# Kernel tuning notes

Measured on AMD Instinct MI355X. Metric: run time of the kernel, lower is better.

The kernel has to match this reference:

```python
import jax, jax.numpy as jnp
import numpy as np

N_NODES, N_EDGES, N_REL, F_DIM, N_HEAD, N_LAYERS = 20000, 100000, 1000, 128, 4, 4
NEG_SLOPE = 0.2  # PyG GATv2Conv default negative_slope


def _gatv2_layer(x, ea_full, src, dst, Wl, bl, Wr, br, We, att, bias):
    # x: [N, F]; ea_full: [Etot, F] edge attrs (incl. self-loop rows)
    N = x.shape[0]
    H, C = att.shape  # heads, out-dim per head
    xl = (x @ Wl + bl).reshape(N, H, C)          # source-side projection
    xr = (x @ Wr + br).reshape(N, H, C)          # target-side projection
    ee = (ea_full @ We).reshape(-1, H, C)        # [Etot, H, C] edge embedding
    # GATv2 scoring: leaky_relu(x_i + x_j + e) . att
    e = jax.nn.leaky_relu(xl[src] + xr[dst] + ee, NEG_SLOPE)
    logits = jnp.einsum('ehc,hc->eh', e, att)    # [Etot, H]
    # segment softmax over edges grouped by destination node
    m = jax.ops.segment_max(logits, dst, num_segments=N)
    p = jnp.exp(logits - m[dst])
    denom = jax.ops.segment_sum(p, dst, num_segments=N)
    alpha = p / denom[dst]                       # [Etot, H]
    out = jax.ops.segment_sum(alpha[:, :, None] * xl[src], dst, num_segments=N)
    return out.mean(axis=1) + bias               # concat=False -> head mean


def setup_inputs() -> dict:
    key = jax.random.key(0)
    ks = jax.random.split(key, 12)
    N, E, R, F, H, L = N_NODES, N_EDGES, N_REL, F_DIM, N_HEAD, N_LAYERS
    HC = H * F
    s = 1.0 / np.sqrt(F)
    return {
        'x': jax.random.normal(ks[0], (N, F), jnp.float32),
        'edge_index': jax.random.randint(ks[1], (2, E), 0, N, dtype=jnp.int32),
        'relations': jax.random.normal(ks[2], (R, F), jnp.float32),
        'relation_index': jax.random.randint(ks[3], (E,), 0, R, dtype=jnp.int32),
        'Wl': jax.random.normal(ks[4], (L, F, HC), jnp.float32) * s,
        'bl': jnp.zeros((L, HC), jnp.float32),
        'Wr': jax.random.normal(ks[5], (L, F, HC), jnp.float32) * s,
        'br': jnp.zeros((L, HC), jnp.float32),
        'We': jax.random.normal(ks[6], (L, F, HC), jnp.float32) * s,
        'att': jax.random.normal(ks[7], (L, H, F), jnp.float32) * s,
        'bias': jnp.zeros((L, F), jnp.float32),
    }


def reference(x, edge_index, relations, relation_index, Wl, bl, Wr, br, We, att, bias):
    N = x.shape[0]
    sl = jnp.arange(N, dtype=edge_index.dtype)
    src = jnp.concatenate([edge_index[0], sl])   # add_self_loops=True
    dst = jnp.concatenate([edge_index[1], sl])
    ea = relations[relation_index]               # [E, F]
    # self-loop edge_attr uses fill_value='mean' (PyG default)
    ea_mean = ea.mean(axis=0)
    ea_full = jnp.concatenate([ea, jnp.broadcast_to(ea_mean, (N, ea.shape[1]))])
    h = x
    for l in range(N_LAYERS):
        h = _gatv2_layer(h, ea_full, src, dst, Wl[l], bl[l], Wr[l], br[l], We[l], att[l], bias[l])
    return (h, relations)
```

## Files before the change

kernel.cpp:

```cpp
#include <hip/hip_runtime.h>
#include <hip/hip_bf16.h>

#define N_NODES   20000
#define N_EDGES   100000
#define N_REL     1000
#define F_DIM     128
#define N_HEAD    4
#define HC        512
#define HC2       256
#define N_LAYERS  4
#define REL_EXT_ROWS 1008
#define NEG_SLOPE 0.2f
#define NODE_MB   ((N_NODES + 63) / 64)
#define REL_MB    ((REL_EXT_ROWS + 63) / 64)

typedef __attribute__((ext_vector_type(8))) short short8;
typedef __attribute__((ext_vector_type(4))) float floatx4;

__device__ __forceinline__ float loadIn(const void* p, size_t i, int f32) {
    if (f32) return ((const float*)p)[i];
    union { unsigned int u; float f; } c;
    c.u = ((unsigned int)((const unsigned short*)p)[i]) << 16;
    return c.f;
}

__device__ __forceinline__ unsigned short f2bf(float v) {
    __hip_bfloat16 b = __float2bfloat16(v);
    return *(unsigned short*)&b;
}

__device__ __forceinline__ void unpack2(unsigned int u, float& lo, float& hi) {
    union { unsigned int u; float f; } a, b;
    a.u = u << 16;
    b.u = u & 0xFFFF0000u;
    lo = a.f; hi = b.f;
}

__device__ __forceinline__ void unpack8(uint4 v, float* f) {
    unpack2(v.x, f[0], f[1]);
    unpack2(v.y, f[2], f[3]);
    unpack2(v.z, f[4], f[5]);
    unpack2(v.w, f[6], f[7]);
}

__global__ void detect_kernel(const unsigned short* __restrict__ x, int* __restrict__ flag) {
    int t = threadIdx.x;
    int cnt = 0;
    for (int j = t; j < 256; j += 64) {
        int e = (x[j] >> 7) & 0xFF;
        if (e >= 143) cnt++;
    }
    for (int off = 32; off; off >>= 1) cnt += __shfl_xor(cnt, off);
    if (t == 0) flag[0] = (cnt >= 8) ? 1 : 0;
}


__global__ void hist_kernel(const int* __restrict__ dst, const int* __restrict__ rel,
                            int* __restrict__ deg, int* __restrict__ rcount) {
    int e = blockIdx.x * 256 + threadIdx.x;
    if (e < N_EDGES) {
        atomicAdd(&deg[dst[e]], 1);
        atomicAdd(&rcount[rel[e]], 1);
    }
}

__global__ void ea_mean_kernel(const int* __restrict__ rcount,
                               const void* __restrict__ relations,
                               float* __restrict__ ea_mean, const int* __restrict__ flag) {
    int f32 = flag[0];
    int b = blockIdx.x;
    int t = threadIdx.x;
    int col = t & 127;
    int rhalf = t >> 7;
    float acc = 0.f;
    for (int j = 0; j < 4; ++j) {
        int r = b * 8 + j * 2 + rhalf;
        acc += (float)rcount[r] * loadIn(relations, (size_t)r * F_DIM + col, f32);
    }
    __shared__ float part[256];
    part[t] = acc;
    __syncthreads();
    if (t < 128)
        atomicAdd(&ea_mean[col], (part[t] + part[t + 128]) * (1.f / (float)N_EDGES));
}

__global__ void relext_kernel(const void* __restrict__ relations,
                              const float* __restrict__ ea_mean,
                              unsigned short* __restrict__ rel_ext, const int* __restrict__ flag) {
    int idx = blockIdx.x * 256 + threadIdx.x;
    if (idx >= REL_EXT_ROWS * F_DIM) return;
    int f32 = flag[0];
    int r = idx >> 7;
    int c = idx & 127;
    float v;
    if (r < N_REL)       v = loadIn(relations, idx, f32);
    else if (r == N_REL) v = ea_mean[c];
    else                 v = 0.f;
    rel_ext[idx] = f2bf(v);
}

__global__ void scan_kernel(const int* __restrict__ deg,
                            int* __restrict__ row_start, int* __restrict__ cursor) {
    __shared__ int part[1024];
    int t = threadIdx.x;
    const int CH = (N_NODES + 1023) / 1024;
    int base = t * CH;
    int sum = 0;
    for (int j = 0; j < CH; ++j) {
        int idx = base + j;
        if (idx < N_NODES) sum += deg[idx];
    }
    part[t] = sum;
    __syncthreads();
    for (int off = 1; off < 1024; off <<= 1) {
        int u = (t >= off) ? part[t - off] : 0;
        __syncthreads();
        part[t] += u;
        __syncthreads();
    }
    int run = part[t] - sum;
    for (int j = 0; j < CH; ++j) {
        int idx = base + j;
        if (idx < N_NODES) {
            row_start[idx] = run;
            cursor[idx] = run;
            run += deg[idx];
        }
    }
    if (t == 1023) row_start[N_NODES] = part[1023];
}

__global__ void scatter_kernel(const int* __restrict__ src, const int* __restrict__ dst,
                               const int* __restrict__ rel, int* __restrict__ cursor,
                               int* __restrict__ csr_pack) {
    int e = blockIdx.x * 256 + threadIdx.x;
    if (e < N_EDGES) {
        int d = dst[e];
        int p = atomicAdd(&cursor[d], 1);
        csr_pack[p] = src[e] | (rel[e] << 16);
    }
}

__global__ void tail_kernel(const void* __restrict__ relations, void* __restrict__ out,
                            const int* __restrict__ flag) {
    int i = blockIdx.x * 256 + threadIdx.x;
    if (i >= N_REL * F_DIM) return;
    int f32 = flag[0];
    float v = loadIn(relations, i, f32);
    size_t o = (size_t)N_NODES * F_DIM + i;
    if (f32) ((float*)out)[o] = v;
    else     ((unsigned short*)out)[o] = f2bf(v);
}

__global__ void w_transpose_kernel(const void* __restrict__ Wl, const void* __restrict__ Wr,
                                   const void* __restrict__ We,
                                   unsigned short* __restrict__ Wt, const int* __restrict__ flag) {
    int f32 = flag[0];
    int k0 = blockIdx.x * 64;
    int n0 = blockIdx.y * 64;
    int mat = blockIdx.z;
    const void* src = (mat < 4) ? Wl : (mat < 8 ? Wr : We);
    size_t base = (size_t)(mat & 3) * F_DIM * HC;
    unsigned short* dst = Wt + (size_t)mat * HC * F_DIM;
    __shared__ float T[64][65];
    int t = threadIdx.x;
    int r = t >> 2, cq = t & 3;
    for (int j = 0; j < 16; ++j) {
        int n = cq * 16 + j;
        T[n][r] = loadIn(src, base + (size_t)(k0 + r) * HC + n0 + n, f32);
    }
    __syncthreads();
    for (int j = 0; j < 16; ++j) {
        int k = cq * 16 + j;
        dst[(size_t)(n0 + r) * F_DIM + k0 + k] = f2bf(T[r][k]);
    }
}

__launch_bounds__(256, 4)
__global__ void proj_kernel(const void* __restrict__ A_node, int a_input,
                            const unsigned short* __restrict__ rel_ext,
                            const unsigned short* __restrict__ Wlt,
                            const unsigned short* __restrict__ Wrt,
                            const unsigned short* __restrict__ Wet,
                            const void* __restrict__ bl, const void* __restrict__ br,
                            size_t boff,
                            unsigned short* __restrict__ xl,
                            unsigned short* __restrict__ xr,
                            unsigned short* __restrict__ re,
                            const int* __restrict__ flag) {
    __shared__ __align__(16) short As[64][136];
    __shared__ __align__(16) short BtRaw[128 * 72];
    int f32 = flag[0];
    int isNode = (blockIdx.x < NODE_MB);
    int m0 = (isNode ? blockIdx.x : (blockIdx.x - NODE_MB)) * 64;
    int M = isNode ? N_NODES : REL_EXT_ROWS;
    int tpb = isNode ? 2 : 1;
    int a_f32 = (isNode && a_input) ? f32 : 0;
    const void* A = isNode ? A_node : (const void*)rel_ext;
    int t = threadIdx.x;

    for (int j = 0; j < 4; ++j) {
        int c = t + j * 256;
        int row = c >> 4;
        int colc = (c & 15) * 8;
        int gm = m0 + row;
        short8 v = (short8){0, 0, 0, 0, 0, 0, 0, 0};
        if (gm < M) {
            size_t idx = (size_t)gm * F_DIM + colc;
            if (a_f32) {
                const float* Af = (const float*)A;
                for (int q = 0; q < 8; ++q) v[q] = (short)f2bf(Af[idx + q]);
            } else {
                v = *(const short8*)((const unsigned short*)A + idx);
            }
        }
        *(short8*)&As[row][colc] = v;
    }

    int wave = t >> 6, lane = t & 63;
    int wm = (wave >> 1) * 32, wn = (wave & 1) * 64;
    int r16 = lane & 15, quad = lane >> 4;

    for (int it = 0; it < tpb; ++it) {
        int nt = isNode ? (blockIdx.y * 2 + it) : blockIdx.y;
        const unsigned short* Wt = isNode ? ((nt < 4) ? Wlt : Wrt) : Wet;
        int n0 = (nt & 3) * 128;

        floatx4 acc[2][4];
        for (int mi = 0; mi < 2; ++mi)
            for (int ni = 0; ni < 4; ++ni)
                acc[mi][ni] = (floatx4){0.f, 0.f, 0.f, 0.f};

        for (int half = 0; half < 2; ++half) {
            __syncthreads();
            for (int j = 0; j < 4; ++j) {
                int c = t + j * 256;
                int nl = c >> 3;
                int kc = (c & 7) * 8;
                *(short8*)&BtRaw[nl * 72 + kc] =
                    *(const short8*)(Wt + (size_t)(n0 + nl) * F_DIM + half * 64 + kc);
            }
            __syncthreads();

            for (int kk = 0; kk < 2; ++kk) {
                short8 a[2], b[4];
                for (int mi = 0; mi < 2; ++mi)
                    a[mi] = *(const short8*)&As[wm + mi * 16 + r16][half * 64 + kk * 32 + quad * 8];
                for (int ni = 0; ni < 4; ++ni)
                    b[ni] = *(const short8*)&BtRaw[(wn + ni * 16 + r16) * 72 + kk * 32 + quad * 8];
                for (int mi = 0; mi < 2; ++mi)
                    for (int ni = 0; ni < 4; ++ni)
                        acc[mi][ni] = __builtin_amdgcn_mfma_f32_16x16x32_bf16(a[mi], b[ni], acc[mi][ni], 0, 0, 0);
            }
        }

        const void* bias = isNode ? ((nt < 4) ? bl : br) : nullptr;
        unsigned short* out = isNode ? ((nt < 4) ? xl : xr) : re;
        __syncthreads();
        for (int mi = 0; mi < 2; ++mi) {
            for (int ni = 0; ni < 4; ++ni) {
                int col = wn + ni * 16 + r16;
                float bv = bias ? loadIn(bias, boff + n0 + col, f32) : 0.f;
                for (int r = 0; r < 4; ++r) {
                    int rowl = wm + mi * 16 + quad * 4 + r;
                    BtRaw[rowl * 136 + col] = (short)f2bf(acc[mi][ni][r] + bv);
                }
            }
        }
        __syncthreads();
        for (int j = 0; j < 4; ++j) {
            int c = t + j * 256;
            int rowl = c >> 4;
            int colc = (c & 15) * 8;
            int gm = m0 + rowl;
            if (gm < M)
                *(short8*)(out + (size_t)gm * HC + n0 + colc) =
                    *(const short8*)&BtRaw[rowl * 136 + colc];
        }
    }
}

__launch_bounds__(256)
__global__ void edge_kernel(const unsigned int* __restrict__ xl2,
                            const unsigned int* __restrict__ xr2,
                            const unsigned int* __restrict__ re2,
                            const int* __restrict__ row_start,
                            const int* __restrict__ csr_pack,
                            const void* __restrict__ att, size_t att_off,
                            const void* __restrict__ bias, size_t bias_off,
                            void* __restrict__ hout, int final_layer,
                            const int* __restrict__ flag) {
    int f32 = flag[0];
    int wid = threadIdx.x >> 6;
    int lane = threadIdx.x & 63;
    int i = blockIdx.x * 4 + wid;
    if (i >= N_NODES) return;
    int h = lane >> 4;
    int q = lane & 15;
    int loff = h * 64 + q * 4;

    float xr[8];
    { uint4 v = *(const uint4*)(xr2 + (size_t)i * HC2 + loff); unpack8(v, xr); }
    float er[8];
    { uint4 v = *(const uint4*)(re2 + (size_t)N_REL * HC2 + loff); unpack8(v, er); }
    float av[8];
    #pragma unroll
    for (int j = 0; j < 8; ++j)
        av[j] = loadIn(att, att_off + (size_t)h * F_DIM + q * 8 + j, f32);

    float acc[8];
    float s;
    {
        float xs[8];
        uint4 v = *(const uint4*)(xl2 + (size_t)i * HC2 + loff);
        unpack8(v, xs);
        float part = 0.f;
        #pragma unroll
        for (int j = 0; j < 8; ++j) {
            float u = xs[j] + xr[j] + er[j];
            u = fmaxf(u, NEG_SLOPE * u);
            part = fmaf(u, av[j], part);
        }
        #pragma unroll
        for (int off = 8; off; off >>= 1) part += __shfl_xor(part, off);
        part = fminf(fmaxf(part, -60.f), 60.f);
        float p = __expf(part);
        s = p;
        #pragma unroll
        for (int j = 0; j < 8; ++j) acc[j] = p * xs[j];
    }

    int e0 = row_start[i], e1 = row_start[i + 1];
    if (e0 < 0) e0 = 0;
    if (e1 > N_EDGES) e1 = N_EDGES;
    if (e1 < e0) e1 = e0;

    for (int b = e0; b < e1; b += 4) {
        int nb = e1 - b; if (nb > 4) nb = 4;
        uint4 xv[4], rv[4];
        #pragma unroll
        for (int k = 0; k < 4; ++k) {
            if (k < nb) {
                int pk = csr_pack[b + k];
                int sn = pk & 0xFFFF;        if (sn >= N_NODES) sn = 0;
                int rn = (pk >> 16) & 0x3FF; if (rn > N_REL) rn = N_REL;
                xv[k] = *(const uint4*)(xl2 + (size_t)sn * HC2 + loff);
                rv[k] = *(const uint4*)(re2 + (size_t)rn * HC2 + loff);
            }
        }
        #pragma unroll
        for (int k = 0; k < 4; ++k) {
            if (k < nb) {
                float xlv[8], ee[8];
                unpack8(xv[k], xlv);
                unpack8(rv[k], ee);
                float part = 0.f;
                #pragma unroll
                for (int j = 0; j < 8; ++j) {
                    float u = xlv[j] + xr[j] + ee[j];
                    u = fmaxf(u, NEG_SLOPE * u);
                    part = fmaf(u, av[j], part);
                }
                #pragma unroll
                for (int off = 8; off; off >>= 1) part += __shfl_xor(part, off);
                part = fminf(fmaxf(part, -60.f), 60.f);
                float pp = __expf(part);
                s += pp;
                #pragma unroll
                for (int j = 0; j < 8; ++j) acc[j] = fmaf(pp, xlv[j], acc[j]);
            }
        }
    }

    float inv = 1.f / s;
    float outv[8];
    #pragma unroll
    for (int j = 0; j < 8; ++j) outv[j] = acc[j] * inv;
    #pragma unroll
    for (int j = 0; j < 8; ++j) {
        outv[j] += __shfl_xor(outv[j], 16);
        outv[j] += __shfl_xor(outv[j], 32);
    }

    if (h == 0) {
        float bv[8];
        #pragma unroll
        for (int j = 0; j < 8; ++j)
            bv[j] = loadIn(bias, bias_off + q * 8 + j, f32);
        size_t o = (size_t)i * F_DIM + q * 8;
        if (final_layer && f32) {
            float* op = (float*)hout + o;
            float4 lo, hi;
            lo.x = outv[0] * 0.25f + bv[0];
            lo.y = outv[1] * 0.25f + bv[1];
            lo.z = outv[2] * 0.25f + bv[2];
            lo.w = outv[3] * 0.25f + bv[3];
            hi.x = outv[4] * 0.25f + bv[4];
            hi.y = outv[5] * 0.25f + bv[5];
            hi.z = outv[6] * 0.25f + bv[6];
            hi.w = outv[7] * 0.25f + bv[7];
            *(float4*)op = lo;
            *(float4*)(op + 4) = hi;
        } else {
            unsigned int w[4];
            #pragma unroll
            for (int p = 0; p < 4; ++p) {
                float v0 = outv[2 * p] * 0.25f + bv[2 * p];
                float v1 = outv[2 * p + 1] * 0.25f + bv[2 * p + 1];
                w[p] = (unsigned int)f2bf(v0) | ((unsigned int)f2bf(v1) << 16);
            }
            *(uint4*)((unsigned short*)hout + o) = *(uint4*)w;
        }
    }
}


extern "C" void kernel_launch(void* const* d_in, const int* in_sizes, int n_in,
                              void* d_out, int out_size, void* d_ws, size_t ws_size,
                              hipStream_t stream) {
    const void* x          = d_in[0];
    const int*  edge_index = (const int*)d_in[1];
    const void* relations  = d_in[2];
    const int*  rel_index  = (const int*)d_in[3];
    const void* Wl         = d_in[4];
    const void* bl         = d_in[5];
    const void* Wr         = d_in[6];
    const void* br         = d_in[7];
    const void* We         = d_in[8];
    const void* att        = d_in[9];
    const void* bias       = d_in[10];

    char* ws = (char*)d_ws;
    size_t off = 0;
    auto alloc = [&](size_t bytes) -> void* {
        void* p = ws + off;
        off = (off + bytes + 255) & ~(size_t)255;
        return p;
    };
    int*            flag     = (int*)alloc(4);
    char*           zero0    = ws + off;
    int*            deg      = (int*)alloc(N_NODES * 4);
    int*            rcount   = (int*)alloc(N_REL * 4);
    float*          ea_mean  = (float*)alloc(F_DIM * 4);
    size_t          zlen     = (size_t)((ws + off) - zero0);
    int*            row_start= (int*)alloc((N_NODES + 1) * 4);
    int*            cursor   = (int*)alloc(N_NODES * 4);
    int*            csr_pack = (int*)alloc(N_EDGES * 4);
    unsigned short* rel_ext  = (unsigned short*)alloc((size_t)REL_EXT_ROWS * F_DIM * 2);
    unsigned short* Wt       = (unsigned short*)alloc((size_t)12 * HC * F_DIM * 2);
    unsigned short* re       = (unsigned short*)alloc((size_t)REL_EXT_ROWS * HC * 2);
    unsigned short* hbuf     = (unsigned short*)alloc((size_t)N_NODES * F_DIM * 2);
    unsigned short* xl       = (unsigned short*)alloc((size_t)N_NODES * HC * 2);
    unsigned short* xr       = (unsigned short*)alloc((size_t)N_NODES * HC * 2);

    const int* esrc = edge_index;
    const int* edst = edge_index + N_EDGES;

    detect_kernel<<<1, 64, 0, stream>>>((const unsigned short*)x, flag);
    hipMemsetAsync(zero0, 0, zlen, stream);
    hist_kernel<<<(N_EDGES + 255) / 256, 256, 0, stream>>>(edst, rel_index, deg, rcount);
    ea_mean_kernel<<<N_REL / 8, 256, 0, stream>>>(rcount, relations, ea_mean, flag);
    relext_kernel<<<(REL_EXT_ROWS * F_DIM + 255) / 256, 256, 0, stream>>>(relations, ea_mean, rel_ext, flag);
    scan_kernel<<<1, 1024, 0, stream>>>(deg, row_start, cursor);
    scatter_kernel<<<(N_EDGES + 255) / 256, 256, 0, stream>>>(esrc, edst, rel_index, cursor, csr_pack);
    w_transpose_kernel<<<dim3(2, 8, 12), 256, 0, stream>>>(Wl, Wr, We, Wt, flag);
    tail_kernel<<<(N_REL * F_DIM + 255) / 256, 256, 0, stream>>>(relations, d_out, flag);

    const void* hin = x;
    int a_input = 1;
    for (int l = 0; l < N_LAYERS; ++l) {
        const unsigned short* Wlt = Wt + (size_t)l * HC * F_DIM;
        const unsigned short* Wrt = Wt + (size_t)(4 + l) * HC * F_DIM;
        const unsigned short* Wet = Wt + (size_t)(8 + l) * HC * F_DIM;
        proj_kernel<<<dim3(NODE_MB + REL_MB, 4), 256, 0, stream>>>(
            hin, a_input, rel_ext, Wlt, Wrt, Wet,
            bl, br, (size_t)l * HC,
            xl, xr, re, flag);
        int final_layer = (l == N_LAYERS - 1);
        void* hout = final_layer ? d_out : (void*)hbuf;
        edge_kernel<<<(N_NODES + 3) / 4, 256, 0, stream>>>(
            (const unsigned int*)xl, (const unsigned int*)xr, (const unsigned int*)re,
            row_start, csr_pack,
            att, (size_t)l * N_HEAD * F_DIM,
            bias, (size_t)l * F_DIM,
            hout, final_layer, flag);
        hin = hbuf;
        a_input = 0;
    }
}
```

Baseline: 444.8 us.

## Pack per-node header with first seven edges and prefetch all their gathers upfront

Adds a setup kernel that builds a 32-byte per-node record holding the row start, the degree and the first seven packed edge entries. The edge kernel loads this record with two vector loads and issues all gathers for up to seven neighbours before any compute, removing the serial row_start then csr_pack then gather dependency chain. Edges beyond seven fall back to the old loop. Blocks shrink to two waves each. This raises register pressure from seven in-flight uint4 pairs and adds one small kernel plus extra workspace.

```diff
diff --git a/kernel.cpp b/kernel.cpp
--- a/kernel.cpp
+++ b/kernel.cpp
@@ -139,6 +139,21 @@
         int p = atomicAdd(&cursor[d], 1);
         csr_pack[p] = src[e] | (rel[e] << 16);
     }
+}
+
+__global__ void build8_kernel(const int* __restrict__ row_start,
+                              const int* __restrict__ csr_pack,
+                              int* __restrict__ csr8) {
+    int i = blockIdx.x * 256 + threadIdx.x;
+    if (i >= N_NODES) return;
+    int rs = row_start[i];
+    int deg = row_start[i + 1] - rs;
+    if (deg < 0) deg = 0;
+    int dcap = deg > 4095 ? 4095 : deg;
+    csr8[i * 8] = rs | (dcap << 17);
+    #pragma unroll
+    for (int k = 0; k < 7; ++k)
+        csr8[i * 8 + 1 + k] = (k < deg) ? csr_pack[rs + k] : 0;
 }
 
 __global__ void tail_kernel(const void* __restrict__ relations, void* __restrict__ out,
@@ -280,11 +295,11 @@
     }
 }
 
-__launch_bounds__(256)
+__launch_bounds__(128)
 __global__ void edge_kernel(const unsigned int* __restrict__ xl2,
                             const unsigned int* __restrict__ xr2,
                             const unsigned int* __restrict__ re2,
-                            const int* __restrict__ row_start,
+                            const int* __restrict__ csr8,
                             const int* __restrict__ csr_pack,
                             const void* __restrict__ att, size_t att_off,
                             const void* __restrict__ bias, size_t bias_off,
@@ -293,11 +308,17 @@
     int f32 = flag[0];
     int wid = threadIdx.x >> 6;
     int lane = threadIdx.x & 63;
-    int i = blockIdx.x * 4 + wid;
+    int i = blockIdx.x * 2 + wid;
     if (i >= N_NODES) return;
     int h = lane >> 4;
     int q = lane & 15;
     int loff = h * 64 + q * 4;
+
+    uint4 h0 = *(const uint4*)(csr8 + (size_t)i * 8);
+    uint4 h1 = *(const uint4*)(csr8 + (size_t)i * 8 + 4);
+    int rs  = (int)(h0.x & 0x1FFFF);
+    int deg = (int)(h0.x >> 17) & 0xFFF;
+    int ew[7] = { (int)h0.y, (int)h0.z, (int)h0.w, (int)h1.x, (int)h1.y, (int)h1.z, (int)h1.w };
 
     float xr[8];
     { uint4 v = *(const uint4*)(xr2 + (size_t)i * HC2 + loff); unpack8(v, xr); }
@@ -307,6 +328,19 @@
     #pragma unroll
     for (int j = 0; j < 8; ++j)
         av[j] = loadIn(att, att_off + (size_t)h * F_DIM + q * 8 + j, f32);
+
+    int nIn = deg > 7 ? 7 : deg;
+    uint4 xv[7], rv[7];
+    #pragma unroll
+    for (int k = 0; k < 7; ++k) {
+        if (k < nIn) {
+            int pk = ew[k];
+            int sn = pk & 0xFFFF;        if (sn >= N_NODES) sn = 0;
+            int rn = (pk >> 16) & 0x3FF; if (rn > N_REL) rn = N_REL;
+            xv[k] = *(const uint4*)(xl2 + (size_t)sn * HC2 + loff);
+            rv[k] = *(const uint4*)(re2 + (size_t)rn * HC2 + loff);
+        }
+    }
 
     float acc[8];
     float s;
@@ -330,44 +364,66 @@
         for (int j = 0; j < 8; ++j) acc[j] = p * xs[j];
     }
 
-    int e0 = row_start[i], e1 = row_start[i + 1];
-    if (e0 < 0) e0 = 0;
-    if (e1 > N_EDGES) e1 = N_EDGES;
-    if (e1 < e0) e1 = e0;
-
-    for (int b = e0; b < e1; b += 4) {
-        int nb = e1 - b; if (nb > 4) nb = 4;
-        uint4 xv[4], rv[4];
-        #pragma unroll
-        for (int k = 0; k < 4; ++k) {
-            if (k < nb) {
-                int pk = csr_pack[b + k];
-                int sn = pk & 0xFFFF;        if (sn >= N_NODES) sn = 0;
-                int rn = (pk >> 16) & 0x3FF; if (rn > N_REL) rn = N_REL;
-                xv[k] = *(const uint4*)(xl2 + (size_t)sn * HC2 + loff);
-                rv[k] = *(const uint4*)(re2 + (size_t)rn * HC2 + loff);
-            }
-        }
-        #pragma unroll
-        for (int k = 0; k < 4; ++k) {
-            if (k < nb) {
-                float xlv[8], ee[8];
-                unpack8(xv[k], xlv);
-                unpack8(rv[k], ee);
-                float part = 0.f;
-                #pragma unroll
-                for (int j = 0; j < 8; ++j) {
-                    float u = xlv[j] + xr[j] + ee[j];
-                    u = fmaxf(u, NEG_SLOPE * u);
-                    part = fmaf(u, av[j], part);
+    #pragma unroll
+    for (int k = 0; k < 7; ++k) {
+        if (k < nIn) {
+            float xlv[8], ee[8];
+            unpack8(xv[k], xlv);
+            unpack8(rv[k], ee);
+            float part = 0.f;
+            #pragma unroll
+            for (int j = 0; j < 8; ++j) {
+                float u = xlv[j] + xr[j] + ee[j];
+                u = fmaxf(u, NEG_SLOPE * u);
+                part = fmaf(u, av[j], part);
+            }
+            #pragma unroll
+            for (int off = 8; off; off >>= 1) part += __shfl_xor(part, off);
+            part = fminf(fmaxf(part, -60.f), 60.f);
+            float pp = __expf(part);
+            s += pp;
+            #pragma unroll
+            for (int j = 0; j < 8; ++j) acc[j] = fmaf(pp, xlv[j], acc[j]);
+        }
+    }
+
+    if (deg > 7) {
+        int e1 = rs + deg;
+        if (e1 > N_EDGES) e1 = N_EDGES;
+        for (int b = rs + 7; b < e1; b += 4) {
+            int nb = e1 - b; if (nb > 4) nb = 4;
+            uint4 xo[4], ro[4];
+            #pragma unroll
+            for (int k = 0; k < 4; ++k) {
+                if (k < nb) {
+                    int pk = csr_pack[b + k];
+                    int sn = pk & 0xFFFF;        if (sn >= N_NODES) sn = 0;
+                    int rn = (pk >> 16) & 0x3FF; if (rn > N_REL) rn = N_REL;
+                    xo[k] = *(const uint4*)(xl2 + (size_t)sn * HC2 + loff);
+                    ro[k] = *(const uint4*)(re2 + (size_t)rn * HC2 + loff);
                 }
-                #pragma unroll
-                for (int off = 8; off; off >>= 1) part += __shfl_xor(part, off);
-                part = fminf(fmaxf(part, -60.f), 60.f);
-                float pp = __expf(part);
-                s += pp;
-                #pragma unroll
-                for (int j = 0; j < 8; ++j) acc[j] = fmaf(pp, xlv[j], acc[j]);
+            }
+            #pragma unroll
+            for (int k = 0; k < 4; ++k) {
+                if (k < nb) {
+                    float xlv[8], ee[8];
+                    unpack8(xo[k], xlv);
+                    unpack8(ro[k], ee);
+                    float part = 0.f;
+                    #pragma unroll
+                    for (int j = 0; j < 8; ++j) {
+                        float u = xlv[j] + xr[j] + ee[j];
+                        u = fmaxf(u, NEG_SLOPE * u);
+                        part = fmaf(u, av[j], part);
+                    }
+                    #pragma unroll
+                    for (int off = 8; off; off >>= 1) part += __shfl_xor(part, off);
+                    part = fminf(fmaxf(part, -60.f), 60.f);
+                    float pp = __expf(part);
+                    s += pp;
+                    #pragma unroll
+                    for (int j = 0; j < 8; ++j) acc[j] = fmaf(pp, xlv[j], acc[j]);
+                }
             }
         }
     }
@@ -446,6 +502,7 @@
     int*            row_start= (int*)alloc((N_NODES + 1) * 4);
     int*            cursor   = (int*)alloc(N_NODES * 4);
     int*            csr_pack = (int*)alloc(N_EDGES * 4);
+    int*            csr8     = (int*)alloc((size_t)N_NODES * 8 * 4);
     unsigned short* rel_ext  = (unsigned short*)alloc((size_t)REL_EXT_ROWS * F_DIM * 2);
     unsigned short* Wt       = (unsigned short*)alloc((size_t)12 * HC * F_DIM * 2);
     unsigned short* re       = (unsigned short*)alloc((size_t)REL_EXT_ROWS * HC * 2);
@@ -463,6 +520,7 @@
     relext_kernel<<<(REL_EXT_ROWS * F_DIM + 255) / 256, 256, 0, stream>>>(relations, ea_mean, rel_ext, flag);
     scan_kernel<<<1, 1024, 0, stream>>>(deg, row_start, cursor);
     scatter_kernel<<<(N_EDGES + 255) / 256, 256, 0, stream>>>(esrc, edst, rel_index, cursor, csr_pack);
+    build8_kernel<<<(N_NODES + 255) / 256, 256, 0, stream>>>(row_start, csr_pack, csr8);
     w_transpose_kernel<<<dim3(2, 8, 12), 256, 0, stream>>>(Wl, Wr, We, Wt, flag);
     tail_kernel<<<(N_REL * F_DIM + 255) / 256, 256, 0, stream>>>(relations, d_out, flag);
 
@@ -478,9 +536,9 @@
             xl, xr, re, flag);
         int final_layer = (l == N_LAYERS - 1);
         void* hout = final_layer ? d_out : (void*)hbuf;
-        edge_kernel<<<(N_NODES + 3) / 4, 256, 0, stream>>>(
+        edge_kernel<<<(N_NODES + 1) / 2, 128, 0, stream>>>(
             (const unsigned int*)xl, (const unsigned int*)xr, (const unsigned int*)re,
-            row_start, csr_pack,
+            csr8, csr_pack,
             att, (size_t)l * N_HEAD * F_DIM,
             bias, (size_t)l * F_DIM,
             hout, final_layer, flag);
```

Result: faster. 416.8 us (-6.3%).
